# Optimization experiments

Hardware: AMD Instinct MI355X
Metric: run time of the kernel (lower is better)

## Reference

```python
import jax, jax.numpy as jnp
import numpy as np

NUM_EXPERTS = 8
DIM = 2048
BATCH = 8192


def setup_inputs() -> dict:
    key = jax.random.key(0)
    k_x, k_ids, k_w, k_b = jax.random.split(key, 4)
    x = jax.random.normal(k_x, (BATCH, DIM), dtype=jnp.float32)
    cam_pred_ids = jax.random.randint(k_ids, (BATCH,), 0, NUM_EXPERTS, dtype=jnp.int64)
    # torch nn.Linear default init: U(-1/sqrt(in), 1/sqrt(in)); W is [out, in]
    bound = 1.0 / np.sqrt(DIM)
    W = jax.random.uniform(k_w, (NUM_EXPERTS, DIM, DIM), dtype=jnp.float32,
                           minval=-bound, maxval=bound)
    b = jax.random.uniform(k_b, (NUM_EXPERTS, DIM), dtype=jnp.float32,
                           minval=-bound, maxval=bound)
    return {"x": x, "cam_pred_ids": cam_pred_ids, "W": W, "b": b}


def reference(x, cam_pred_ids, W, b):
    # Per-sample expert routing: out[i] = x[i] + relu(x[i] @ W[e].T + b[e]),
    # where e = cam_pred_ids[i]. Vectorized as 8 full-batch GEMMs with masked
    # combine (fixed small expert count -> Python loop is structural, not data).
    h = jnp.zeros_like(x)
    for e in range(NUM_EXPERTS):
        he = jax.nn.relu(x @ W[e].T + b[e])          # [B, D]
        mask = (cam_pred_ids == e)[:, None]
        h = h + jnp.where(mask, he, jnp.zeros((), dtype=x.dtype))
    return x + h
```

## Files before the change

kernel.cpp:

```cpp
#include <hip/hip_runtime.h>
#include <hip/hip_bf16.h>
#include <stdint.h>

#define BATCH 8192
#define DIM   2048
#define NEXP  8
#define BM    128
#define BN    128
#define BK    32
#define NITER (DIM / BK)
#define MAX_TILES 72
#define NBLK  (DIM / BN)
#define NROWS 9216
#define NXBB  2048
#define NCVTB 4096

typedef __bf16 bf16x8 __attribute__((ext_vector_type(8)));
typedef float  f32x4  __attribute__((ext_vector_type(4)));

#define ZP_BYTE_OFF 40960ull
#define XB_BYTE_OFF 49152ull
#define WB_BYTE_OFF 37789696ull
#define WS_NEED     104898560ull

#define AS1(p) ((const __attribute__((address_space(1))) void*)(p))
#define AS3(p) ((__attribute__((address_space(3))) void*)(p))

__device__ __forceinline__ unsigned f2bf2(float lo, float hi) {
    unsigned ul = __float_as_uint(lo), uh = __float_as_uint(hi);
    ul = (ul + 0x7FFFu + ((ul >> 16) & 1u)) >> 16;
    uh = (uh + 0x7FFFu + ((uh >> 16) & 1u)) >> 16;
    return (uh << 16) | ul;
}

__global__ __launch_bounds__(512)
void k_prep(const int* __restrict__ ids, int* __restrict__ ws,
            int* __restrict__ rowmap,
            const float4* __restrict__ x4, uint4* __restrict__ xb4,
            const float4* __restrict__ W, uint4* __restrict__ Wb,
            int* __restrict__ zp) {
    int b = blockIdx.x;
    int t = threadIdx.x;
    if (b > 0) {
        const float4* src; uint4* dst; size_t base;
        if (b <= NXBB) { src = x4; dst = xb4; base = (size_t)(b - 1) * 1024; }
        else           { src = W;  dst = Wb;  base = (size_t)(b - 1 - NXBB) * 1024; }
#pragma unroll
        for (int j = 0; j < 2; j++) {
            size_t o = base + (size_t)j * 512 + t;
            float4 a = src[o * 2], c = src[o * 2 + 1];
            uint4 v;
            v.x = f2bf2(a.x, a.y);  v.y = f2bf2(a.z, a.w);
            v.z = f2bf2(c.x, c.y);  v.w = f2bf2(c.z, c.w);
            dst[o] = v;
        }
        return;
    }
    zp[t] = 0; zp[t + 512] = 0;
    __shared__ int sc[512 * NEXP];
    __shared__ int seg[NEXP];
    __shared__ int tot[NEXP];
    int myids[16];
    int base = t * 16;
#pragma unroll
    for (int e = 0; e < NEXP; e++) sc[t * NEXP + e] = 0;
#pragma unroll
    for (int i = 0; i < 16; i++) {
        myids[i] = ids[base + i];
        sc[t * NEXP + myids[i]]++;
    }
    __syncthreads();
    {
        int w = t >> 6, l = t & 63;
        int e = w;
        int vals[8], sum = 0;
#pragma unroll
        for (int j = 0; j < 8; j++) { vals[j] = sc[(l * 8 + j) * NEXP + e]; sum += vals[j]; }
        int inc = sum;
        for (int d = 1; d < 64; d <<= 1) {
            int v = __shfl_up(inc, d, 64);
            if (l >= d) inc += v;
        }
        int run = inc - sum;
#pragma unroll
        for (int j = 0; j < 8; j++) { int v = vals[j]; sc[(l * 8 + j) * NEXP + e] = run; run += v; }
        if (l == 63) tot[e] = run;
    }
    __syncthreads();
    if (t == 0) {
        int pos = 0, mt = 0;
        for (int e = 0; e < NEXP; e++) {
            int c = tot[e];
            seg[e] = pos;
            int ntl = (c + BM - 1) / BM;
            for (int tt = 0; tt < ntl; tt++) {
                ws[64  + mt] = e;
                ws[160 + mt] = pos + tt * BM;
                int v = c - tt * BM;
                ws[256 + mt] = v < BM ? v : BM;
                mt++;
            }
            pos += ntl * BM;
        }
        ws[48] = mt;
    }
    __syncthreads();
    for (int i = t; i < NROWS; i += 512) rowmap[i] = -1;
    __syncthreads();
#pragma unroll
    for (int i = 0; i < 16; i++) {
        int e = myids[i];
        int p = seg[e] + sc[t * NEXP + e]++;
        rowmap[p] = base + i;
    }
}

__launch_bounds__(256)
__global__ void k_gemm(const float* __restrict__ x,
                       const unsigned short* __restrict__ xb,
                       const unsigned short* __restrict__ Wb,
                       const unsigned short* __restrict__ zp,
                       const float* __restrict__ bias,
                       const int* __restrict__ ws, const int* __restrict__ rowmap,
                       float* __restrict__ out) {
    int nb = blockIdx.x;
    int mt = blockIdx.y;
    if (mt >= ws[48]) return;
    int e     = ws[64  + mt];
    int pos0  = ws[160 + mt];
    int valid = ws[256 + mt];
    int n0 = nb * BN;

    __shared__ unsigned short lds[2][8192];

    int tid = threadIdx.x;
    int w = tid >> 6, l = tid & 63;
    int lane15 = l & 15, quad = l >> 4;
    int wave_m = (w >> 1) * 64, wave_n = (w & 1) * 64;

    const unsigned short* Bbase = Wb + (size_t)e * DIM * DIM + (size_t)n0 * DIM;

    const unsigned short* aptr[2];
    int srcOffB[2];
#pragma unroll
    for (int j = 0; j < 2; j++) {
        int c = w * 128 + j * 64 + l;
        int row = c >> 2, pos = c & 3;
        int q = pos ^ ((row >> 1) & 3);
        int rm = rowmap[pos0 + row];
        const unsigned short* rb = (rm >= 0) ? (xb + (size_t)rm * DIM) : zp;
        aptr[j] = rb + q * 8;
        srcOffB[j] = row * DIM + q * 8;
    }

    int swz = (quad ^ ((lane15 >> 1) & 3)) * 8;
    int afOff[4], bfOff[4];
#pragma unroll
    for (int mi = 0; mi < 4; mi++)
        afOff[mi] = (wave_m + mi * 16 + lane15) * BK + swz;
#pragma unroll
    for (int ni = 0; ni < 4; ni++)
        bfOff[ni] = 4096 + (wave_n + ni * 16 + lane15) * BK + swz;

    f32x4 acc[4][4];
#pragma unroll
    for (int i = 0; i < 4; i++)
#pragma unroll
        for (int j = 0; j < 4; j++) acc[i][j] = (f32x4){0.f, 0.f, 0.f, 0.f};

#define ISSUE(buf, k0)                                                          \
    do {                                                                        \
        _Pragma("unroll")                                                       \
        for (int j = 0; j < 2; j++) {                                           \
            __builtin_amdgcn_global_load_lds(                                   \
                AS1(aptr[j] + (k0)),                                            \
                AS3(&lds[buf][w * 1024 + j * 512]), 16, 0, 0);                  \
            __builtin_amdgcn_global_load_lds(                                   \
                AS1(Bbase + (k0) + srcOffB[j]),                                 \
                AS3(&lds[buf][4096 + w * 1024 + j * 512]), 16, 0, 0);           \
        }                                                                       \
    } while (0)

    ISSUE(0, 0);
    int cur = 0;
    for (int i = 0; i < NITER; ++i) {
        __syncthreads();
        if (i + 1 < NITER) {
            int k0n = (i + 1) * BK;
            ISSUE(cur ^ 1, k0n);
        }
        bf16x8 af[4], bf[4];
#pragma unroll
        for (int mi = 0; mi < 4; mi++)
            af[mi] = *(const bf16x8*)(&lds[cur][afOff[mi]]);
#pragma unroll
        for (int ni = 0; ni < 4; ni++)
            bf[ni] = *(const bf16x8*)(&lds[cur][bfOff[ni]]);
#pragma unroll
        for (int mi = 0; mi < 4; mi++)
#pragma unroll
            for (int ni = 0; ni < 4; ni++)
                acc[mi][ni] = __builtin_amdgcn_mfma_f32_16x16x32_bf16(
                    af[mi], bf[ni], acc[mi][ni], 0, 0, 0);
        cur ^= 1;
    }
#undef ISSUE

    float bv[4];
#pragma unroll
    for (int ni = 0; ni < 4; ni++)
        bv[ni] = bias[(size_t)e * DIM + n0 + wave_n + ni * 16 + lane15];
#pragma unroll
    for (int mi = 0; mi < 4; mi++) {
#pragma unroll
        for (int r4 = 0; r4 < 4; r4++) {
            int rl = wave_m + mi * 16 + quad * 4 + r4;
            if (rl < valid) {
                int orig = rowmap[pos0 + rl];
                const float* xrow = x + (size_t)orig * DIM + n0;
                float* orow = out + (size_t)orig * DIM + n0;
#pragma unroll
                for (int ni = 0; ni < 4; ni++) {
                    int col = wave_n + ni * 16 + lane15;
                    float v = acc[mi][ni][r4] + bv[ni];
                    v = v > 0.f ? v : 0.f;
                    orow[col] = xrow[col] + v;
                }
            }
        }
    }
}

__global__ void k_naive(const float* __restrict__ x, const int* __restrict__ ids,
                        const float* __restrict__ W, const float* __restrict__ b,
                        float* __restrict__ out) {
    __shared__ float lx[DIM];
    int i = blockIdx.x;
    for (int t = threadIdx.x; t < DIM; t += blockDim.x) lx[t] = x[(size_t)i * DIM + t];
    __syncthreads();
    int e = ids[i];
    const float* We = W + (size_t)e * DIM * DIM;
    for (int n = threadIdx.x; n < DIM; n += blockDim.x) {
        const float* wr = We + (size_t)n * DIM;
        float acc = 0.f;
        for (int k = 0; k < DIM; k += 4) {
            float4 w4 = *(const float4*)(wr + k);
            acc += lx[k] * w4.x + lx[k + 1] * w4.y + lx[k + 2] * w4.z + lx[k + 3] * w4.w;
        }
        float v = acc + b[(size_t)e * DIM + n];
        v = v > 0.f ? v : 0.f;
        out[(size_t)i * DIM + n] = lx[n] + v;
    }
}

extern "C" void kernel_launch(void* const* d_in, const int* in_sizes, int n_in,
                              void* d_out, int out_size, void* d_ws, size_t ws_size,
                              hipStream_t stream) {
    const float* x   = (const float*)d_in[0];
    const int*   ids = (const int*)d_in[1];
    const float* W   = (const float*)d_in[2];
    const float* b   = (const float*)d_in[3];
    float* out = (float*)d_out;

    if (ws_size < WS_NEED) {
        k_naive<<<BATCH, 256, 0, stream>>>(x, ids, W, b, out);
        return;
    }

    char* wsb = (char*)d_ws;
    int*  wsi = (int*)wsb;
    int* rowmap = wsi + 512;
    int* zp = (int*)(wsb + ZP_BYTE_OFF);
    unsigned short* xb = (unsigned short*)(wsb + XB_BYTE_OFF);
    unsigned short* Wb = (unsigned short*)(wsb + WB_BYTE_OFF);

    k_prep<<<1 + NXBB + NCVTB, 512, 0, stream>>>(ids, wsi, rowmap,
                                                 (const float4*)x, (uint4*)xb,
                                                 (const float4*)W, (uint4*)Wb, zp);
    dim3 g(NBLK, MAX_TILES);
    k_gemm<<<g, 256, 0, stream>>>(x, xb, Wb, (const unsigned short*)zp,
                                  b, wsi, rowmap, out);
}
```

Measured before the change: 407.6 us.

## Pre-gather x rows into an expert-sorted bf16 buffer and reuse it for the residual

Routing is planned in a separate single-block kernel. The prep kernel then writes x, converted to bf16, into a contiguous expert-sorted buffer, with padded rows zero-filled, while also converting W with more work per block. The GEMM loads A tiles from this contiguous buffer instead of indirecting through rowmap per row. The epilogue reads the residual x from the bf16 buffer instead of fp32 x, which halves that traffic but adds rounding error to the output and an extra serialized launch.

```diff
diff --git a/kernel.cpp b/kernel.cpp
--- a/kernel.cpp
+++ b/kernel.cpp
@@ -12,14 +12,13 @@
 #define MAX_TILES 72
 #define NBLK  (DIM / BN)
 #define NROWS 9216
-#define NXBB  2048
-#define NCVTB 4096
+#define XROWB 2304
+#define WCVTB 2048
 
 typedef __bf16 bf16x8 __attribute__((ext_vector_type(8)));
 typedef float  f32x4  __attribute__((ext_vector_type(4)));
 
-#define ZP_BYTE_OFF 40960ull
-#define XB_BYTE_OFF 49152ull
+#define XG_BYTE_OFF 40960ull
 #define WB_BYTE_OFF 37789696ull
 #define WS_NEED     104898560ull
 
@@ -34,32 +33,12 @@
 }
 
 __global__ __launch_bounds__(512)
-void k_prep(const int* __restrict__ ids, int* __restrict__ ws,
-            int* __restrict__ rowmap,
-            const float4* __restrict__ x4, uint4* __restrict__ xb4,
-            const float4* __restrict__ W, uint4* __restrict__ Wb,
-            int* __restrict__ zp) {
-    int b = blockIdx.x;
-    int t = threadIdx.x;
-    if (b > 0) {
-        const float4* src; uint4* dst; size_t base;
-        if (b <= NXBB) { src = x4; dst = xb4; base = (size_t)(b - 1) * 1024; }
-        else           { src = W;  dst = Wb;  base = (size_t)(b - 1 - NXBB) * 1024; }
-#pragma unroll
-        for (int j = 0; j < 2; j++) {
-            size_t o = base + (size_t)j * 512 + t;
-            float4 a = src[o * 2], c = src[o * 2 + 1];
-            uint4 v;
-            v.x = f2bf2(a.x, a.y);  v.y = f2bf2(a.z, a.w);
-            v.z = f2bf2(c.x, c.y);  v.w = f2bf2(c.z, c.w);
-            dst[o] = v;
-        }
-        return;
-    }
-    zp[t] = 0; zp[t + 512] = 0;
+void k_plan(const int* __restrict__ ids, int* __restrict__ ws,
+            int* __restrict__ rowmap) {
     __shared__ int sc[512 * NEXP];
     __shared__ int seg[NEXP];
     __shared__ int tot[NEXP];
+    int t = threadIdx.x;
     int myids[16];
     int base = t * 16;
 #pragma unroll
@@ -115,21 +94,53 @@
     }
 }
 
+__global__ __launch_bounds__(512)
+void k_prep(const float* __restrict__ x, const int* __restrict__ rowmap,
+            unsigned short* __restrict__ xg,
+            const float4* __restrict__ W, uint4* __restrict__ Wb) {
+    int b = blockIdx.x;
+    int t = threadIdx.x;
+    if (b < XROWB) {
+        int rm[4];
+#pragma unroll
+        for (int r = 0; r < 4; r++) rm[r] = rowmap[b * 4 + r];
+#pragma unroll
+        for (int r = 0; r < 4; r++) {
+            int row = b * 4 + r;
+            uint2* o = (uint2*)(xg + (size_t)row * DIM);
+            if (rm[r] < 0) { o[t] = make_uint2(0, 0); continue; }
+            float4 a = ((const float4*)(x + (size_t)rm[r] * DIM))[t];
+            uint2 v;
+            v.x = f2bf2(a.x, a.y);
+            v.y = f2bf2(a.z, a.w);
+            o[t] = v;
+        }
+        return;
+    }
+    size_t base = (size_t)(b - XROWB) * 2048;
+#pragma unroll
+    for (int j = 0; j < 4; j++) {
+        size_t o = base + (size_t)j * 512 + t;
+        float4 a = W[o * 2], c = W[o * 2 + 1];
+        uint4 v;
+        v.x = f2bf2(a.x, a.y);  v.y = f2bf2(a.z, a.w);
+        v.z = f2bf2(c.x, c.y);  v.w = f2bf2(c.z, c.w);
+        Wb[o] = v;
+    }
+}
+
 __launch_bounds__(256)
-__global__ void k_gemm(const float* __restrict__ x,
-                       const unsigned short* __restrict__ xb,
+__global__ void k_gemm(const unsigned short* __restrict__ xg,
                        const unsigned short* __restrict__ Wb,
-                       const unsigned short* __restrict__ zp,
                        const float* __restrict__ bias,
                        const int* __restrict__ ws, const int* __restrict__ rowmap,
                        float* __restrict__ out) {
-    int nb = blockIdx.x;
     int mt = blockIdx.y;
     if (mt >= ws[48]) return;
     int e     = ws[64  + mt];
     int pos0  = ws[160 + mt];
     int valid = ws[256 + mt];
-    int n0 = nb * BN;
+    int n0 = blockIdx.x * BN;
 
     __shared__ unsigned short lds[2][8192];
 
@@ -138,19 +149,16 @@
     int lane15 = l & 15, quad = l >> 4;
     int wave_m = (w >> 1) * 64, wave_n = (w & 1) * 64;
 
+    const unsigned short* Abase = xg + (size_t)pos0 * DIM;
     const unsigned short* Bbase = Wb + (size_t)e * DIM * DIM + (size_t)n0 * DIM;
 
-    const unsigned short* aptr[2];
-    int srcOffB[2];
+    int srcOff[2];
 #pragma unroll
     for (int j = 0; j < 2; j++) {
         int c = w * 128 + j * 64 + l;
         int row = c >> 2, pos = c & 3;
         int q = pos ^ ((row >> 1) & 3);
-        int rm = rowmap[pos0 + row];
-        const unsigned short* rb = (rm >= 0) ? (xb + (size_t)rm * DIM) : zp;
-        aptr[j] = rb + q * 8;
-        srcOffB[j] = row * DIM + q * 8;
+        srcOff[j] = row * DIM + q * 8;
     }
 
     int swz = (quad ^ ((lane15 >> 1) & 3)) * 8;
@@ -173,10 +181,10 @@
         _Pragma("unroll")                                                       \
         for (int j = 0; j < 2; j++) {                                           \
             __builtin_amdgcn_global_load_lds(                                   \
-                AS1(aptr[j] + (k0)),                                            \
+                AS1(Abase + (k0) + srcOff[j]),                                  \
                 AS3(&lds[buf][w * 1024 + j * 512]), 16, 0, 0);                  \
             __builtin_amdgcn_global_load_lds(                                   \
-                AS1(Bbase + (k0) + srcOffB[j]),                                 \
+                AS1(Bbase + (k0) + srcOff[j]),                                  \
                 AS3(&lds[buf][4096 + w * 1024 + j * 512]), 16, 0, 0);           \
         }                                                                       \
     } while (0)
@@ -217,14 +225,15 @@
             int rl = wave_m + mi * 16 + quad * 4 + r4;
             if (rl < valid) {
                 int orig = rowmap[pos0 + rl];
-                const float* xrow = x + (size_t)orig * DIM + n0;
+                const unsigned short* xrow = xg + (size_t)(pos0 + rl) * DIM + n0;
                 float* orow = out + (size_t)orig * DIM + n0;
 #pragma unroll
                 for (int ni = 0; ni < 4; ni++) {
                     int col = wave_n + ni * 16 + lane15;
+                    float xv = __uint_as_float((unsigned)xrow[col] << 16);
                     float v = acc[mi][ni][r4] + bv[ni];
                     v = v > 0.f ? v : 0.f;
-                    orow[col] = xrow[col] + v;
+                    orow[col] = xv + v;
                 }
             }
         }
@@ -270,14 +279,12 @@
     char* wsb = (char*)d_ws;
     int*  wsi = (int*)wsb;
     int* rowmap = wsi + 512;
-    int* zp = (int*)(wsb + ZP_BYTE_OFF);
-    unsigned short* xb = (unsigned short*)(wsb + XB_BYTE_OFF);
+    unsigned short* xg = (unsigned short*)(wsb + XG_BYTE_OFF);
     unsigned short* Wb = (unsigned short*)(wsb + WB_BYTE_OFF);
 
-    k_prep<<<1 + NXBB + NCVTB, 512, 0, stream>>>(ids, wsi, rowmap,
-                                                 (const float4*)x, (uint4*)xb,
-                                                 (const float4*)W, (uint4*)Wb, zp);
+    k_plan<<<1, 512, 0, stream>>>(ids, wsi, rowmap);
+    k_prep<<<XROWB + WCVTB, 512, 0, stream>>>(x, rowmap, xg,
+                                              (const float4*)W, (uint4*)Wb);
     dim3 g(NBLK, MAX_TILES);
-    k_gemm<<<g, 256, 0, stream>>>(x, xb, Wb, (const unsigned short*)zp,
-                                  b, wsi, rowmap, out);
-}
+    k_gemm<<<g, 256, 0, stream>>>(xg, Wb, b, wsi, rowmap, out);
+}
```

Result: faster. 396.9 us (-2.6%).
